# Kernel optimization log

Measured on AMD Instinct MI355X. Metric: run time of the kernel, lower is better.

## Reference

```python
import jax, jax.numpy as jnp
import numpy as np
from jax.ops import segment_sum

N_NODES = 50000
N_EDGES = 800000
D_IN = 256
D_HID2 = 256   # hidden_channels * 2
D_HID = 128    # hidden_channels
D_MLP = 64     # hidden_channels // 2
D_OUT = 64


def setup_inputs() -> dict:
    key = jax.random.key(0)
    ks = jax.random.split(key, 16)
    def glorot(k, shape):
        lim = float(np.sqrt(6.0 / (shape[0] + shape[1])))
        return jax.random.uniform(k, shape, jnp.float32, -lim, lim)
    x = jax.random.normal(ks[0], (N_NODES, D_IN), jnp.float32)
    edge_index = jax.random.randint(ks[1], (2, N_EDGES), 0, N_NODES, jnp.int64)
    return {
        "x": x,
        "edge_index": edge_index,
        "W1": glorot(ks[2], (D_IN, D_HID2)),   "b1": jnp.zeros((D_HID2,), jnp.float32),
        "W2": glorot(ks[3], (D_HID2, D_HID2)), "b2": jnp.zeros((D_HID2,), jnp.float32),
        "W3": glorot(ks[4], (D_HID2, D_HID)),  "b3": jnp.zeros((D_HID,), jnp.float32),
        "mW1": glorot(ks[5], (D_HID, D_MLP)),  "mb1": jnp.zeros((D_MLP,), jnp.float32),
        "mW2": glorot(ks[6], (D_MLP, D_OUT)),  "mb2": jnp.zeros((D_OUT,), jnp.float32),
    }


def _graph_conv(x, src, dst, W, b, n_nodes):
    # DGL GraphConv with norm='both': h = D_in^{-1/2} * A @ (D_out^{-1/2} * x @ W) + b
    ones = jnp.ones((src.shape[0],), x.dtype)
    deg_out = jnp.clip(segment_sum(ones, src, num_segments=n_nodes), 1.0)
    deg_in = jnp.clip(segment_sum(ones, dst, num_segments=n_nodes), 1.0)
    h = (x * jax.lax.rsqrt(deg_out)[:, None]) @ W          # [N, d_out]
    agg = segment_sum(h[src], dst, num_segments=n_nodes)    # gather-scatter over edges
    return agg * jax.lax.rsqrt(deg_in)[:, None] + b


def reference(x, edge_index, W1, b1, W2, b2, W3, b3, mW1, mb1, mW2, mb2):
    src, dst = edge_index[0], edge_index[1]
    n = x.shape[0]
    # eval mode: dropout is identity
    h = jax.nn.relu(_graph_conv(x, src, dst, W1, b1, n))
    h = jax.nn.relu(_graph_conv(h, src, dst, W2, b2, n))
    h_last = jax.nn.relu(_graph_conv(h, src, dst, W3, b3, n))
    out = jax.nn.relu(h_last @ mW1 + mb1) @ mW2 + mb2
    return (out, h_last)
```

## Files before the change

### kernel.cpp

```cpp
#include <hip/hip_runtime.h>
#include <hip/hip_bf16.h>

typedef __hip_bfloat16 bf16;
typedef __attribute__((ext_vector_type(8))) __bf16 bfrag;
typedef __attribute__((ext_vector_type(4))) float f32x4;

#define N_NODES 50000
#define N_EDGES 800000
#define GB_GEMM 782
#define GB_PLACE 3125

__device__ __forceinline__ unsigned short f2bf(float f) {
    bf16 h = __float2bfloat16(f);
    return *reinterpret_cast<unsigned short*>(&h);
}

__device__ __forceinline__ uint4 zero4() { uint4 z; z.x = z.y = z.z = z.w = 0u; return z; }

__device__ __forceinline__ void load_edge(const int* __restrict__ ei, int fl64,
                                          int e, int& s, int& d) {
    if (fl64) { s = ei[2 * e]; d = ei[2 * N_EDGES + 2 * e]; }
    else      { s = ei[e];     d = ei[N_EDGES + e]; }
}

__device__ __forceinline__ float rdf(const void* p, int off, int f32) {
    return f32 ? ((const float*)p)[off] : (float)((const bf16*)p)[off];
}

__global__ void detect_zero_kernel(const unsigned short* __restrict__ xb,
                                   const int* __restrict__ ei,
                                   int* __restrict__ flags,
                                   int* __restrict__ cnt) {
    int i = blockIdx.x * 256 + threadIdx.x;
    if (i < 2 * N_NODES) cnt[i] = 0;
    if (blockIdx.x == 0) {
        __shared__ int s_insane, s_nonzero;
        int t = threadIdx.x;
        if (t == 0) { s_insane = 0; s_nonzero = 0; }
        __syncthreads();
        unsigned short h = xb[2 * t];
        int e = (h >> 7) & 0xFF;
        if (!(e == 0 || (e >= 90 && e <= 150))) atomicOr(&s_insane, 1);
        if (ei[2 * t + 1] != 0) atomicOr(&s_nonzero, 1);
        __syncthreads();
        if (t == 0) { flags[0] = s_insane ? 1 : 0; flags[1] = s_nonzero ? 0 : 1; }
    }
}

__global__ void cvt_all_kernel(const void* W1, const void* W2, const void* W3,
                               const void* mW1, const void* mW2,
                               const void* b1, const void* b2, const void* b3,
                               const void* mb1, const void* mb2,
                               const int* __restrict__ flags,
                               unsigned short* __restrict__ WT,
                               float* __restrict__ biasd) {
    int i = blockIdx.x * 256 + threadIdx.x;
    if (i >= 176896) return;
    const int f32 = flags[0];
    if (i < 163840) {
        const void* s; int local, N;
        if      (i <  65536) { s = W1; local = i;          N = 256; }
        else if (i < 131072) { s = W2; local = i -  65536; N = 256; }
        else                 { s = W3; local = i - 131072; N = 128; }
        int n = local >> 8, k = local & 255;
        WT[i] = f2bf(rdf(s, k * N + n, f32));
    } else if (i < 172032) {
        int local = i - 163840;
        int n = local >> 7, k = local & 127;
        WT[i] = f2bf(rdf(mW1, k * 64 + n, f32));
    } else if (i < 176128) {
        int local = i - 172032;
        int n = local >> 6, k = local & 63;
        WT[i] = f2bf(rdf(mW2, k * 64 + n, f32));
    } else {
        int local = i - 176128;
        const void* s; int off;
        if      (local < 256) { s = b1;  off = local; }
        else if (local < 512) { s = b2;  off = local - 256; }
        else if (local < 640) { s = b3;  off = local - 512; }
        else if (local < 704) { s = mb1; off = local - 640; }
        else                  { s = mb2; off = local - 704; }
        biasd[local] = rdf(s, off, f32);
    }
}

__device__ __forceinline__ uint4 ld8_bf16(const unsigned short* p) {
    return *(const uint4*)p;
}
__device__ __forceinline__ uint4 ld8_f32(const float* p) {
    float4 a = *(const float4*)(p);
    float4 b = *(const float4*)(p + 4);
    uint4 r;
    r.x = ((unsigned)f2bf(a.y) << 16) | f2bf(a.x);
    r.y = ((unsigned)f2bf(a.w) << 16) | f2bf(a.z);
    r.z = ((unsigned)f2bf(b.y) << 16) | f2bf(b.x);
    r.w = ((unsigned)f2bf(b.w) << 16) | f2bf(b.z);
    return r;
}

template <bool DUALX>
__device__ __forceinline__ void gemm_body(
        unsigned short (*Xs)[40], unsigned short (*Ws)[40],
        const void* __restrict__ Xv, const int* __restrict__ flags,
        const unsigned short* __restrict__ WT,
        unsigned short* __restrict__ C,
        int bx, int by, int M, int N) {
    constexpr int K = 256;
    const int tid  = threadIdx.x;
    const int lane = tid & 63;
    const int w    = tid >> 6;
    const int wr   = (w >> 1) * 64;
    const int wc   = (w & 1) * 64;
    const int lrow = lane & 15;
    const int koff = (lane >> 4) * 8;
    const int row0 = by * 128;
    const int col0 = bx * 128;
    const bool xf32 = DUALX && (flags[0] != 0);
    const unsigned short* Xb = (const unsigned short*)Xv;
    const float* Xf = (const float*)Xv;

    const int r0 = tid >> 2, q0 = tid & 3;
    const int r1 = r0 + 64;
    const int gr0 = row0 + r0, gr1 = row0 + r1;

    uint4 xv0, xv1, wv0, wv1;
    {
        int e = q0 * 8;
        xv0 = (gr0 < M) ? (xf32 ? ld8_f32(Xf + (size_t)gr0 * K + e)
                                : ld8_bf16(Xb + (size_t)gr0 * K + e)) : zero4();
        xv1 = (gr1 < M) ? (xf32 ? ld8_f32(Xf + (size_t)gr1 * K + e)
                                : ld8_bf16(Xb + (size_t)gr1 * K + e)) : zero4();
        wv0 = *(const uint4*)(WT + (size_t)(col0 + r0) * K + e);
        wv1 = *(const uint4*)(WT + (size_t)(col0 + r1) * K + e);
    }

    f32x4 acc[4][4] = {};

    for (int k0 = 0; k0 < K; k0 += 32) {
        *(uint4*)&Xs[r0][q0 * 8] = xv0;
        *(uint4*)&Xs[r1][q0 * 8] = xv1;
        *(uint4*)&Ws[r0][q0 * 8] = wv0;
        *(uint4*)&Ws[r1][q0 * 8] = wv1;
        __syncthreads();

        const int k1 = k0 + 32;
        if (k1 < K) {
            int e = k1 + q0 * 8;
            xv0 = (gr0 < M) ? (xf32 ? ld8_f32(Xf + (size_t)gr0 * K + e)
                                    : ld8_bf16(Xb + (size_t)gr0 * K + e)) : zero4();
            xv1 = (gr1 < M) ? (xf32 ? ld8_f32(Xf + (size_t)gr1 * K + e)
                                    : ld8_bf16(Xb + (size_t)gr1 * K + e)) : zero4();
            wv0 = *(const uint4*)(WT + (size_t)(col0 + r0) * K + e);
            wv1 = *(const uint4*)(WT + (size_t)(col0 + r1) * K + e);
        }

        bfrag af[4], bv[4];
#pragma unroll
        for (int i = 0; i < 4; i++)
            af[i] = *(const bfrag*)&Xs[wr + i * 16 + lrow][koff];
#pragma unroll
        for (int j = 0; j < 4; j++)
            bv[j] = *(const bfrag*)&Ws[wc + j * 16 + lrow][koff];
#pragma unroll
        for (int i = 0; i < 4; i++)
#pragma unroll
            for (int j = 0; j < 4; j++)
                acc[i][j] = __builtin_amdgcn_mfma_f32_16x16x32_bf16(
                    af[i], bv[j], acc[i][j], 0, 0, 0);
        __syncthreads();
    }

#pragma unroll
    for (int i = 0; i < 4; i++) {
#pragma unroll
        for (int r = 0; r < 4; r++) {
            int row = row0 + wr + i * 16 + ((lane >> 4) * 4) + r;
            if (row >= M) continue;
#pragma unroll
            for (int j = 0; j < 4; j++) {
                int col = col0 + wc + j * 16 + lrow;
                C[(size_t)row * N + col] = f2bf(acc[i][j][r]);
            }
        }
    }
}

__launch_bounds__(256)
__global__ void megaA_kernel(const void* __restrict__ x,
                             const int* __restrict__ ei,
                             const int* __restrict__ flags,
                             const unsigned short* __restrict__ WT,
                             unsigned short* __restrict__ Hbf,
                             int* __restrict__ cntS, int* __restrict__ cntD,
                             unsigned short* __restrict__ esrc_pad, int M) {
    __shared__ unsigned short Xs[128][40];
    __shared__ unsigned short Ws[128][40];
    const int bid = blockIdx.x;
    if (bid < GB_GEMM) {
        gemm_body<true>(Xs, Ws, x, flags, WT, Hbf, bid & 1, bid >> 1, M, 256);
    } else {
        int e = (bid - GB_GEMM) * 256 + threadIdx.x;
        if (e < N_EDGES) {
            int s, d; load_edge(ei, flags[1], e, s, d);
            atomicAdd(&cntS[s], 1);
            int pos = atomicAdd(&cntD[d], 1);
            if (pos < 64) esrc_pad[(d << 6) + pos] = (unsigned short)s;
        }
    }
}

__launch_bounds__(256)
__global__ void mfma_gemm_kernel(const unsigned short* __restrict__ X,
                                 const int* __restrict__ flags,
                                 const unsigned short* __restrict__ WT,
                                 unsigned short* __restrict__ C,
                                 int M, int N) {
    __shared__ unsigned short Xs[128][40];
    __shared__ unsigned short Ws[128][40];
    gemm_body<false>(Xs, Ws, X, flags, WT, C, blockIdx.x, blockIdx.y, M, N);
}

__launch_bounds__(256)
__global__ void mfma_mlp2_kernel(const unsigned short* __restrict__ X,
                                 const unsigned short* __restrict__ WT1,
                                 const unsigned short* __restrict__ WT2,
                                 const float* __restrict__ b1,
                                 const float* __restrict__ b2,
                                 float* __restrict__ out, int M) {
    __shared__ unsigned short Xs[128][136];
    __shared__ unsigned short W1s[64][136];
    __shared__ unsigned short W2s[64][72];
    const int tid  = threadIdx.x;
    const int lane = tid & 63;
    const int w    = tid >> 6;
    const int lrow = lane & 15;
    const int koff = (lane >> 4) * 8;
    const int row0 = blockIdx.x * 128;

#pragma unroll
    for (int i = 0; i < 8; i++) {
        int c = tid + i * 256;
        int r = c >> 4, q = c & 15;
        int gr = row0 + r;
        uint4 v = (gr < M) ? *(const uint4*)(X + (size_t)gr * 128 + q * 8) : zero4();
        *(uint4*)&Xs[r][q * 8] = v;
    }
#pragma unroll
    for (int i = 0; i < 4; i++) {
        int c = tid + i * 256;
        int n = c >> 4, q = c & 15;
        *(uint4*)&W1s[n][q * 8] = *(const uint4*)(WT1 + (size_t)n * 128 + q * 8);
    }
#pragma unroll
    for (int i = 0; i < 2; i++) {
        int c = tid + i * 256;
        int n = c >> 3, q = c & 7;
        *(uint4*)&W2s[n][q * 8] = *(const uint4*)(WT2 + (size_t)n * 64 + q * 8);
    }
    __syncthreads();

    f32x4 acc[2][4] = {};
#pragma unroll
    for (int k0 = 0; k0 < 128; k0 += 32) {
        bfrag af[2], bv[4];
#pragma unroll
        for (int i = 0; i < 2; i++)
            af[i] = *(const bfrag*)&Xs[w * 32 + i * 16 + lrow][k0 + koff];
#pragma unroll
        for (int j = 0; j < 4; j++)
            bv[j] = *(const bfrag*)&W1s[j * 16 + lrow][k0 + koff];
#pragma unroll
        for (int i = 0; i < 2; i++)
#pragma unroll
            for (int j = 0; j < 4; j++)
                acc[i][j] = __builtin_amdgcn_mfma_f32_16x16x32_bf16(
                    af[i], bv[j], acc[i][j], 0, 0, 0);
    }
    __syncthreads();

#pragma unroll
    for (int i = 0; i < 2; i++) {
#pragma unroll
        for (int r = 0; r < 4; r++) {
            int row = w * 32 + i * 16 + ((lane >> 4) * 4) + r;
#pragma unroll
            for (int j = 0; j < 4; j++) {
                int col = j * 16 + lrow;
                Xs[row][col] = f2bf(fmaxf(acc[i][j][r] + b1[col], 0.0f));
            }
        }
    }
    __syncthreads();

    f32x4 acc2[2][4] = {};
#pragma unroll
    for (int k0 = 0; k0 < 64; k0 += 32) {
        bfrag af[2], bv[4];
#pragma unroll
        for (int i = 0; i < 2; i++)
            af[i] = *(const bfrag*)&Xs[w * 32 + i * 16 + lrow][k0 + koff];
#pragma unroll
        for (int j = 0; j < 4; j++)
            bv[j] = *(const bfrag*)&W2s[j * 16 + lrow][k0 + koff];
#pragma unroll
        for (int i = 0; i < 2; i++)
#pragma unroll
            for (int j = 0; j < 4; j++)
                acc2[i][j] = __builtin_amdgcn_mfma_f32_16x16x32_bf16(
                    af[i], bv[j], acc2[i][j], 0, 0, 0);
    }

#pragma unroll
    for (int i = 0; i < 2; i++) {
#pragma unroll
        for (int r = 0; r < 4; r++) {
            int row = row0 + w * 32 + i * 16 + ((lane >> 4) * 4) + r;
            if (row >= M) continue;
#pragma unroll
            for (int j = 0; j < 4; j++) {
                int col = j * 16 + lrow;
                out[(size_t)row * 64 + col] = acc2[i][j][r] + b2[col];
            }
        }
    }
}

__device__ __forceinline__ void accs(unsigned int u, float s, float& a0, float& a1) {
    a0 = fmaf(s, __uint_as_float(u << 16), a0);
    a1 = fmaf(s, __uint_as_float(u & 0xffff0000u), a1);
}
__device__ __forceinline__ void acc4s(uint4 u, float s, float& a0, float& a1,
                                      float& a2, float& a3, float& a4, float& a5,
                                      float& a6, float& a7) {
    accs(u.x, s, a0, a1); accs(u.y, s, a2, a3);
    accs(u.z, s, a4, a5); accs(u.w, s, a6, a7);
}

template <int LQ, int OUT>
__launch_bounds__(256)
__global__ void gather_bf16_kernel(const int* __restrict__ cntD,
                                   const int* __restrict__ cntS,
                                   const unsigned short* __restrict__ esrc_pad,
                                   const unsigned short* __restrict__ H,
                                   const float* __restrict__ bias,
                                   float* __restrict__ Yf,
                                   unsigned short* __restrict__ Yb, int nNodes) {
    constexpr int NPB = 256 / LQ;
    constexpr int D = LQ * 8;
    const int tid = threadIdx.x;
    const int node = blockIdx.x * NPB + tid / LQ;
    const int lane = tid % LQ;
    if (node >= nNodes) return;
    const uint4* __restrict__ H4 = (const uint4*)H;
    const unsigned short* __restrict__ ep = esrc_pad + (node << 6);

    float a0 = 0.f, a1 = 0.f, a2 = 0.f, a3 = 0.f;
    float a4 = 0.f, a5 = 0.f, a6 = 0.f, a7 = 0.f;
    const int cn = min(cntD[node], 64);
    int j = 0;
    for (; j + 4 <= cn; j += 4) {
        int s0 = ep[j], s1 = ep[j + 1], s2 = ep[j + 2], s3 = ep[j + 3];
        float w0 = rsqrtf((float)max(cntS[s0], 1));
        float w1 = rsqrtf((float)max(cntS[s1], 1));
        float w2 = rsqrtf((float)max(cntS[s2], 1));
        float w3 = rsqrtf((float)max(cntS[s3], 1));
        uint4 u0 = H4[(size_t)s0 * LQ + lane];
        uint4 u1 = H4[(size_t)s1 * LQ + lane];
        uint4 u2 = H4[(size_t)s2 * LQ + lane];
        uint4 u3 = H4[(size_t)s3 * LQ + lane];
        acc4s(u0, w0, a0, a1, a2, a3, a4, a5, a6, a7);
        acc4s(u1, w1, a0, a1, a2, a3, a4, a5, a6, a7);
        acc4s(u2, w2, a0, a1, a2, a3, a4, a5, a6, a7);
        acc4s(u3, w3, a0, a1, a2, a3, a4, a5, a6, a7);
    }
    for (; j < cn; j++) {
        int s0 = ep[j];
        float w0 = rsqrtf((float)max(cntS[s0], 1));
        uint4 u = H4[(size_t)s0 * LQ + lane];
        acc4s(u, w0, a0, a1, a2, a3, a4, a5, a6, a7);
    }
    const float sc = rsqrtf((float)max(cntD[node], 1));
    const float* bp = bias + lane * 8;
    float4 b0 = *(const float4*)(bp);
    float4 b1 = *(const float4*)(bp + 4);
    float r0 = fmaxf(fmaf(a0, sc, b0.x), 0.0f);
    float r1 = fmaxf(fmaf(a1, sc, b0.y), 0.0f);
    float r2 = fmaxf(fmaf(a2, sc, b0.z), 0.0f);
    float r3 = fmaxf(fmaf(a3, sc, b0.w), 0.0f);
    float r4 = fmaxf(fmaf(a4, sc, b1.x), 0.0f);
    float r5 = fmaxf(fmaf(a5, sc, b1.y), 0.0f);
    float r6 = fmaxf(fmaf(a6, sc, b1.z), 0.0f);
    float r7 = fmaxf(fmaf(a7, sc, b1.w), 0.0f);
    if (OUT == 2) {
        float* yp = Yf + (size_t)node * D + lane * 8;
        float4 o0 = {r0, r1, r2, r3};
        float4 o1 = {r4, r5, r6, r7};
        *(float4*)(yp)     = o0;
        *(float4*)(yp + 4) = o1;
    }
    {
        unsigned short* yp = Yb + (size_t)node * D + lane * 8;
        ushort4 o0, o1;
        o0.x = f2bf(r0); o0.y = f2bf(r1); o0.z = f2bf(r2); o0.w = f2bf(r3);
        o1.x = f2bf(r4); o1.y = f2bf(r5); o1.z = f2bf(r6); o1.w = f2bf(r7);
        *(ushort4*)(yp)     = o0;
        *(ushort4*)(yp + 4) = o1;
    }
}

extern "C" void kernel_launch(void* const* d_in, const int* in_sizes, int n_in,
                              void* d_out, int out_size, void* d_ws, size_t ws_size,
                              hipStream_t stream) {
    const void* x  = d_in[0];
    const int*  ei = (const int*)d_in[1];
    const void *W1 = d_in[2],  *b1 = d_in[3];
    const void *W2 = d_in[4],  *b2 = d_in[5];
    const void *W3 = d_in[6],  *b3 = d_in[7];
    const void *mW1 = d_in[8], *mb1 = d_in[9];
    const void *mW2 = d_in[10],*mb2 = d_in[11];

    float* out   = (float*)d_out;
    float* out_h = out + (size_t)N_NODES * 64;

    float* ws = (float*)d_ws;
    size_t off = 0;
    int*   flags  = (int*)(ws + off); off += 64;
    int*   cntS   = (int*)(ws + off); off += N_NODES;
    int*   cntD   = (int*)(ws + off); off += N_NODES;
    unsigned short* esrc_p = (unsigned short*)(ws + off);
    off += (size_t)N_NODES * 32;
    float* biasd  = ws + off;         off += 768;
    off = (off + 63) & ~(size_t)63;
    unsigned short* WT  = (unsigned short*)(ws + off); off += 88448;
    unsigned short* Gbf = (unsigned short*)(ws + off); off += (size_t)N_NODES * 128;
    unsigned short* Hbf = (unsigned short*)(ws + off); off += (size_t)N_NODES * 128;
    unsigned short* hob = (unsigned short*)(ws + off); off += (size_t)N_NODES * 64;

    const int M = N_NODES;
    const dim3 blk(256);
    const int gy128 = (M + 127) / 128;

    detect_zero_kernel<<<391, blk, 0, stream>>>(
        (const unsigned short*)x, ei, flags, cntS);

    cvt_all_kernel<<<(176896 + 255) / 256, blk, 0, stream>>>(
        W1, W2, W3, mW1, mW2, b1, b2, b3, mb1, mb2, flags, WT, biasd);

    megaA_kernel<<<GB_GEMM + GB_PLACE, blk, 0, stream>>>(
        x, ei, flags, WT, Hbf, cntS, cntD, esrc_p, M);

    gather_bf16_kernel<32, 0><<<(M + 7) / 8, blk, 0, stream>>>(
        cntD, cntS, esrc_p, Hbf, biasd, nullptr, Gbf, M);

    mfma_gemm_kernel<<<dim3(2, gy128), blk, 0, stream>>>(
        Gbf, flags, WT + 65536, Hbf, M, 256);
    gather_bf16_kernel<32, 0><<<(M + 7) / 8, blk, 0, stream>>>(
        cntD, cntS, esrc_p, Hbf, biasd + 256, nullptr, Gbf, M);

    mfma_gemm_kernel<<<dim3(1, gy128), blk, 0, stream>>>(
        Gbf, flags, WT + 131072, Hbf, M, 128);
    gather_bf16_kernel<16, 2><<<(M + 15) / 16, blk, 0, stream>>>(
        cntD, cntS, esrc_p, Hbf, biasd + 512, out_h, hob, M);

    mfma_mlp2_kernel<<<gy128, blk, 0, stream>>>(
        hob, WT + 163840, WT + 172032, biasd + 640, biasd + 704, out, M);
}
```

Before: 382.4 us.

## Sort per-node source lists and precompute degree rsqrt scales for gathers

Adds a kernel that bitonic-sorts each destination node's padded source list within a wavefront, and precomputes rsqrt of the out-degree and in-degree per node into float arrays. The three gather kernels then read those scales instead of recomputing rsqrt from the count arrays. Sorting the sources makes gathered rows follow ascending addresses, which is meant to improve cache and TLB locality. Smaller changes: vectorized int2 edge loads for int64 indices and nontemporal stores for the adjacency writes. The cost is one extra launch and a pass over the padded adjacency.

```diff
diff --git a/kernel.cpp b/kernel.cpp
--- a/kernel.cpp
+++ b/kernel.cpp
@@ -19,8 +19,14 @@
 
 __device__ __forceinline__ void load_edge(const int* __restrict__ ei, int fl64,
                                           int e, int& s, int& d) {
-    if (fl64) { s = ei[2 * e]; d = ei[2 * N_EDGES + 2 * e]; }
-    else      { s = ei[e];     d = ei[N_EDGES + e]; }
+    if (fl64) {
+        int2 a = ((const int2*)ei)[e];
+        int2 b = ((const int2*)ei)[N_EDGES + e];
+        s = a.x; d = b.x;
+    } else {
+        s = ei[e];
+        d = ei[N_EDGES + e];
+    }
 }
 
 __device__ __forceinline__ float rdf(const void* p, int off, int f32) {
@@ -204,8 +210,41 @@
             int s, d; load_edge(ei, flags[1], e, s, d);
             atomicAdd(&cntS[s], 1);
             int pos = atomicAdd(&cntD[d], 1);
-            if (pos < 64) esrc_pad[(d << 6) + pos] = (unsigned short)s;
+            if (pos < 64)
+                __builtin_nontemporal_store((unsigned short)s,
+                                            &esrc_pad[(d << 6) + pos]);
         }
+    }
+}
+
+__launch_bounds__(256)
+__global__ void sort_scale_kernel(const int* __restrict__ cntD,
+                                  const int* __restrict__ cntS,
+                                  unsigned short* __restrict__ esrc_pad,
+                                  float* __restrict__ sOutf,
+                                  float* __restrict__ sInf, int nNodes) {
+    const int node = blockIdx.x * 4 + (threadIdx.x >> 6);
+    const int lane = threadIdx.x & 63;
+    if (node >= nNodes) return;
+    unsigned short* ep = esrc_pad + (node << 6);
+    const int cn = min(cntD[node], 64);
+    unsigned v = (lane < cn) ? (unsigned)ep[lane] : 0xFFFFu;
+#pragma unroll
+    for (int k = 2; k <= 64; k <<= 1) {
+#pragma unroll
+        for (int m = k >> 1; m >= 1; m >>= 1) {
+            unsigned p = __shfl_xor(v, m, 64);
+            bool lower = (lane & m) == 0;
+            bool asc   = (lane & k) == 0;
+            unsigned lo = v < p ? v : p;
+            unsigned hi = v < p ? p : v;
+            v = (asc == lower) ? lo : hi;
+        }
+    }
+    if (lane < cn) ep[lane] = (unsigned short)v;
+    if (lane == 0) {
+        sOutf[node] = rsqrtf((float)max(cntS[node], 1));
+        sInf[node]  = rsqrtf((float)max(cntD[node], 1));
     }
 }
 
@@ -339,10 +378,11 @@
 template <int LQ, int OUT>
 __launch_bounds__(256)
 __global__ void gather_bf16_kernel(const int* __restrict__ cntD,
-                                   const int* __restrict__ cntS,
+                                   const float* __restrict__ sOutf,
                                    const unsigned short* __restrict__ esrc_pad,
                                    const unsigned short* __restrict__ H,
                                    const float* __restrict__ bias,
+                                   const float* __restrict__ sInf,
                                    float* __restrict__ Yf,
                                    unsigned short* __restrict__ Yb, int nNodes) {
     constexpr int NPB = 256 / LQ;
@@ -360,10 +400,10 @@
     int j = 0;
     for (; j + 4 <= cn; j += 4) {
         int s0 = ep[j], s1 = ep[j + 1], s2 = ep[j + 2], s3 = ep[j + 3];
-        float w0 = rsqrtf((float)max(cntS[s0], 1));
-        float w1 = rsqrtf((float)max(cntS[s1], 1));
-        float w2 = rsqrtf((float)max(cntS[s2], 1));
-        float w3 = rsqrtf((float)max(cntS[s3], 1));
+        float w0 = sOutf[s0];
+        float w1 = sOutf[s1];
+        float w2 = sOutf[s2];
+        float w3 = sOutf[s3];
         uint4 u0 = H4[(size_t)s0 * LQ + lane];
         uint4 u1 = H4[(size_t)s1 * LQ + lane];
         uint4 u2 = H4[(size_t)s2 * LQ + lane];
@@ -375,11 +415,11 @@
     }
     for (; j < cn; j++) {
         int s0 = ep[j];
-        float w0 = rsqrtf((float)max(cntS[s0], 1));
+        float w0 = sOutf[s0];
         uint4 u = H4[(size_t)s0 * LQ + lane];
         acc4s(u, w0, a0, a1, a2, a3, a4, a5, a6, a7);
     }
-    const float sc = rsqrtf((float)max(cntD[node], 1));
+    const float sc = sInf[node];
     const float* bp = bias + lane * 8;
     float4 b0 = *(const float4*)(bp);
     float4 b1 = *(const float4*)(bp + 4);
@@ -430,6 +470,8 @@
     unsigned short* esrc_p = (unsigned short*)(ws + off);
     off += (size_t)N_NODES * 32;
     float* biasd  = ws + off;         off += 768;
+    float* sOutf  = ws + off;         off += N_NODES;
+    float* sInf   = ws + off;         off += N_NODES;
     off = (off + 63) & ~(size_t)63;
     unsigned short* WT  = (unsigned short*)(ws + off); off += 88448;
     unsigned short* Gbf = (unsigned short*)(ws + off); off += (size_t)N_NODES * 128;
@@ -449,18 +491,21 @@
     megaA_kernel<<<GB_GEMM + GB_PLACE, blk, 0, stream>>>(
         x, ei, flags, WT, Hbf, cntS, cntD, esrc_p, M);
 
+    sort_scale_kernel<<<(M + 3) / 4, blk, 0, stream>>>(
+        cntD, cntS, esrc_p, sOutf, sInf, M);
+
     gather_bf16_kernel<32, 0><<<(M + 7) / 8, blk, 0, stream>>>(
-        cntD, cntS, esrc_p, Hbf, biasd, nullptr, Gbf, M);
+        cntD, sOutf, esrc_p, Hbf, biasd, sInf, nullptr, Gbf, M);
 
     mfma_gemm_kernel<<<dim3(2, gy128), blk, 0, stream>>>(
         Gbf, flags, WT + 65536, Hbf, M, 256);
     gather_bf16_kernel<32, 0><<<(M + 7) / 8, blk, 0, stream>>>(
-        cntD, cntS, esrc_p, Hbf, biasd + 256, nullptr, Gbf, M);
+        cntD, sOutf, esrc_p, Hbf, biasd + 256, sInf, nullptr, Gbf, M);
 
     mfma_gemm_kernel<<<dim3(1, gy128), blk, 0, stream>>>(
         Gbf, flags, WT + 131072, Hbf, M, 128);
     gather_bf16_kernel<16, 2><<<(M + 15) / 16, blk, 0, stream>>>(
-        cntD, cntS, esrc_p, Hbf, biasd + 512, out_h, hob, M);
+        cntD, sOutf, esrc_p, Hbf, biasd + 512, sInf, out_h, hob, M);
 
     mfma_mlp2_kernel<<<gy128, blk, 0, stream>>>(
         hob, WT + 163840, WT + 172032, biasd + 640, biasd + 704, out, M);
```

Result: slower. 399.0 us (+4.3%).

## Fuse gather-aggregate with next-layer GEMM and MLP into single kernels

Applied to the files above, without the earlier changes.

Each layer's gather/aggregate is merged with the following dense GEMM in one kernel. The aggregated 32-row tile stays in LDS and is multiplied by the next weight matrix, whose rows are then scaled by the source-degree rsqrt so the next gather skips the per-edge cntS lookup. The final conv gather is fused with the two-layer MLP. The edge load uses int2 and the padded-index stores are nontemporal. This removes intermediate global round trips and launches, but the GEMMs now read B fragments straight from global memory in small tiles, which may lower MFMA efficiency.

```diff
diff --git a/kernel.cpp b/kernel.cpp
--- a/kernel.cpp
+++ b/kernel.cpp
@@ -19,8 +19,14 @@
 
 __device__ __forceinline__ void load_edge(const int* __restrict__ ei, int fl64,
                                           int e, int& s, int& d) {
-    if (fl64) { s = ei[2 * e]; d = ei[2 * N_EDGES + 2 * e]; }
-    else      { s = ei[e];     d = ei[N_EDGES + e]; }
+    if (fl64) {
+        int2 a = ((const int2*)ei)[e];
+        int2 b = ((const int2*)ei)[N_EDGES + e];
+        s = a.x; d = b.x;
+    } else {
+        s = ei[e];
+        d = ei[N_EDGES + e];
+    }
 }
 
 __device__ __forceinline__ float rdf(const void* p, int off, int f32) {
@@ -204,207 +210,219 @@
             int s, d; load_edge(ei, flags[1], e, s, d);
             atomicAdd(&cntS[s], 1);
             int pos = atomicAdd(&cntD[d], 1);
-            if (pos < 64) esrc_pad[(d << 6) + pos] = (unsigned short)s;
-        }
-    }
-}
-
-__launch_bounds__(256)
-__global__ void mfma_gemm_kernel(const unsigned short* __restrict__ X,
-                                 const int* __restrict__ flags,
-                                 const unsigned short* __restrict__ WT,
-                                 unsigned short* __restrict__ C,
-                                 int M, int N) {
-    __shared__ unsigned short Xs[128][40];
-    __shared__ unsigned short Ws[128][40];
-    gemm_body<false>(Xs, Ws, X, flags, WT, C, blockIdx.x, blockIdx.y, M, N);
-}
-
-__launch_bounds__(256)
-__global__ void mfma_mlp2_kernel(const unsigned short* __restrict__ X,
-                                 const unsigned short* __restrict__ WT1,
-                                 const unsigned short* __restrict__ WT2,
-                                 const float* __restrict__ b1,
-                                 const float* __restrict__ b2,
-                                 float* __restrict__ out, int M) {
-    __shared__ unsigned short Xs[128][136];
-    __shared__ unsigned short W1s[64][136];
-    __shared__ unsigned short W2s[64][72];
-    const int tid  = threadIdx.x;
+            if (pos < 64)
+                __builtin_nontemporal_store((unsigned short)s,
+                                            &esrc_pad[(d << 6) + pos]);
+        }
+    }
+}
+
+__device__ __forceinline__ void accs(unsigned int u, float s, float& a0, float& a1) {
+    a0 = fmaf(s, __uint_as_float(u << 16), a0);
+    a1 = fmaf(s, __uint_as_float(u & 0xffff0000u), a1);
+}
+__device__ __forceinline__ void acc4s(uint4 u, float s, float (&a)[8]) {
+    accs(u.x, s, a[0], a[1]); accs(u.y, s, a[2], a[3]);
+    accs(u.z, s, a[4], a[5]); accs(u.w, s, a[6], a[7]);
+}
+
+template <int LQ, bool ESCALE>
+__device__ __forceinline__ void gather_accum(const uint4* __restrict__ H4,
+                                             const unsigned short* __restrict__ ep,
+                                             const int* __restrict__ cntS,
+                                             int cn, int lane, float (&a)[8]) {
+    int j = 0;
+    for (; j + 4 <= cn; j += 4) {
+        int s0 = ep[j], s1 = ep[j + 1], s2 = ep[j + 2], s3 = ep[j + 3];
+        float w0 = 1.f, w1 = 1.f, w2 = 1.f, w3 = 1.f;
+        if (ESCALE) {
+            w0 = rsqrtf((float)max(cntS[s0], 1));
+            w1 = rsqrtf((float)max(cntS[s1], 1));
+            w2 = rsqrtf((float)max(cntS[s2], 1));
+            w3 = rsqrtf((float)max(cntS[s3], 1));
+        }
+        uint4 u0 = H4[(size_t)s0 * LQ + lane];
+        uint4 u1 = H4[(size_t)s1 * LQ + lane];
+        uint4 u2 = H4[(size_t)s2 * LQ + lane];
+        uint4 u3 = H4[(size_t)s3 * LQ + lane];
+        acc4s(u0, w0, a); acc4s(u1, w1, a);
+        acc4s(u2, w2, a); acc4s(u3, w3, a);
+    }
+    for (; j < cn; j++) {
+        int s0 = ep[j];
+        float w0 = ESCALE ? rsqrtf((float)max(cntS[s0], 1)) : 1.f;
+        uint4 u = H4[(size_t)s0 * LQ + lane];
+        acc4s(u, w0, a);
+    }
+}
+
+template <int NOUT, bool ESCALE>
+__launch_bounds__(512)
+__global__ void fconv_kernel(const unsigned short* __restrict__ H,
+                             const int* __restrict__ cntD,
+                             const int* __restrict__ cntS,
+                             const unsigned short* __restrict__ esrc_pad,
+                             const float* __restrict__ bias,
+                             const unsigned short* __restrict__ WTn,
+                             unsigned short* __restrict__ Hout,
+                             int M) {
+    __shared__ unsigned short Xf[32][264];
+    const int tid = threadIdx.x;
+    const int row0 = blockIdx.x * 32;
+
+    {
+        const int slot = tid >> 5;
+        const int gl   = tid & 31;
+        const uint4* H4 = (const uint4*)H;
+        const float* bp = bias + gl * 8;
+        float4 b0 = *(const float4*)(bp);
+        float4 b1 = *(const float4*)(bp + 4);
+#pragma unroll
+        for (int round = 0; round < 2; ++round) {
+            const int node = row0 + round * 16 + slot;
+            float a[8] = {};
+            float sc = 0.f;
+            if (node < M) {
+                const unsigned short* ep = esrc_pad + (node << 6);
+                const int cn = min(cntD[node], 64);
+                gather_accum<32, ESCALE>(H4, ep, cntS, cn, gl, a);
+                sc = rsqrtf((float)max(cntD[node], 1));
+            }
+            ushort4 o0, o1;
+            o0.x = f2bf(fmaxf(fmaf(a[0], sc, b0.x), 0.f));
+            o0.y = f2bf(fmaxf(fmaf(a[1], sc, b0.y), 0.f));
+            o0.z = f2bf(fmaxf(fmaf(a[2], sc, b0.z), 0.f));
+            o0.w = f2bf(fmaxf(fmaf(a[3], sc, b0.w), 0.f));
+            o1.x = f2bf(fmaxf(fmaf(a[4], sc, b1.x), 0.f));
+            o1.y = f2bf(fmaxf(fmaf(a[5], sc, b1.y), 0.f));
+            o1.z = f2bf(fmaxf(fmaf(a[6], sc, b1.z), 0.f));
+            o1.w = f2bf(fmaxf(fmaf(a[7], sc, b1.w), 0.f));
+            *(ushort4*)&Xf[round * 16 + slot][gl * 8]     = o0;
+            *(ushort4*)&Xf[round * 16 + slot][gl * 8 + 4] = o1;
+        }
+    }
+    __syncthreads();
+
     const int lane = tid & 63;
     const int w    = tid >> 6;
     const int lrow = lane & 15;
     const int koff = (lane >> 4) * 8;
-    const int row0 = blockIdx.x * 128;
-
-#pragma unroll
-    for (int i = 0; i < 8; i++) {
-        int c = tid + i * 256;
-        int r = c >> 4, q = c & 15;
-        int gr = row0 + r;
-        uint4 v = (gr < M) ? *(const uint4*)(X + (size_t)gr * 128 + q * 8) : zero4();
-        *(uint4*)&Xs[r][q * 8] = v;
-    }
-#pragma unroll
-    for (int i = 0; i < 4; i++) {
-        int c = tid + i * 256;
-        int n = c >> 4, q = c & 15;
-        *(uint4*)&W1s[n][q * 8] = *(const uint4*)(WT1 + (size_t)n * 128 + q * 8);
-    }
-#pragma unroll
-    for (int i = 0; i < 2; i++) {
-        int c = tid + i * 256;
-        int n = c >> 3, q = c & 7;
-        *(uint4*)&W2s[n][q * 8] = *(const uint4*)(WT2 + (size_t)n * 64 + q * 8);
-    }
-    __syncthreads();
-
-    f32x4 acc[2][4] = {};
-#pragma unroll
-    for (int k0 = 0; k0 < 128; k0 += 32) {
-        bfrag af[2], bv[4];
-#pragma unroll
-        for (int i = 0; i < 2; i++)
-            af[i] = *(const bfrag*)&Xs[w * 32 + i * 16 + lrow][k0 + koff];
-#pragma unroll
-        for (int j = 0; j < 4; j++)
-            bv[j] = *(const bfrag*)&W1s[j * 16 + lrow][k0 + koff];
-#pragma unroll
-        for (int i = 0; i < 2; i++)
-#pragma unroll
-            for (int j = 0; j < 4; j++)
-                acc[i][j] = __builtin_amdgcn_mfma_f32_16x16x32_bf16(
-                    af[i], bv[j], acc[i][j], 0, 0, 0);
-    }
-    __syncthreads();
-
-#pragma unroll
-    for (int i = 0; i < 2; i++) {
-#pragma unroll
-        for (int r = 0; r < 4; r++) {
-            int row = w * 32 + i * 16 + ((lane >> 4) * 4) + r;
-#pragma unroll
-            for (int j = 0; j < 4; j++) {
-                int col = j * 16 + lrow;
-                Xs[row][col] = f2bf(fmaxf(acc[i][j][r] + b1[col], 0.0f));
-            }
-        }
-    }
-    __syncthreads();
-
-    f32x4 acc2[2][4] = {};
-#pragma unroll
-    for (int k0 = 0; k0 < 64; k0 += 32) {
-        bfrag af[2], bv[4];
-#pragma unroll
-        for (int i = 0; i < 2; i++)
-            af[i] = *(const bfrag*)&Xs[w * 32 + i * 16 + lrow][k0 + koff];
-#pragma unroll
-        for (int j = 0; j < 4; j++)
-            bv[j] = *(const bfrag*)&W2s[j * 16 + lrow][k0 + koff];
-#pragma unroll
-        for (int i = 0; i < 2; i++)
-#pragma unroll
-            for (int j = 0; j < 4; j++)
-                acc2[i][j] = __builtin_amdgcn_mfma_f32_16x16x32_bf16(
-                    af[i], bv[j], acc2[i][j], 0, 0, 0);
-    }
-
-#pragma unroll
-    for (int i = 0; i < 2; i++) {
-#pragma unroll
-        for (int r = 0; r < 4; r++) {
-            int row = row0 + w * 32 + i * 16 + ((lane >> 4) * 4) + r;
-            if (row >= M) continue;
-#pragma unroll
-            for (int j = 0; j < 4; j++) {
-                int col = j * 16 + lrow;
-                out[(size_t)row * 64 + col] = acc2[i][j][r] + b2[col];
-            }
-        }
-    }
-}
-
-__device__ __forceinline__ void accs(unsigned int u, float s, float& a0, float& a1) {
-    a0 = fmaf(s, __uint_as_float(u << 16), a0);
-    a1 = fmaf(s, __uint_as_float(u & 0xffff0000u), a1);
-}
-__device__ __forceinline__ void acc4s(uint4 u, float s, float& a0, float& a1,
-                                      float& a2, float& a3, float& a4, float& a5,
-                                      float& a6, float& a7) {
-    accs(u.x, s, a0, a1); accs(u.y, s, a2, a3);
-    accs(u.z, s, a4, a5); accs(u.w, s, a6, a7);
-}
-
-template <int LQ, int OUT>
-__launch_bounds__(256)
-__global__ void gather_bf16_kernel(const int* __restrict__ cntD,
-                                   const int* __restrict__ cntS,
-                                   const unsigned short* __restrict__ esrc_pad,
-                                   const unsigned short* __restrict__ H,
-                                   const float* __restrict__ bias,
-                                   float* __restrict__ Yf,
-                                   unsigned short* __restrict__ Yb, int nNodes) {
-    constexpr int NPB = 256 / LQ;
-    constexpr int D = LQ * 8;
+    const int wr   = (w >> 2) * 16;
+    constexpr int NJ = (NOUT == 256) ? 4 : 2;
+    const int wc   = (w & 3) * (NJ * 16);
+    f32x4 acc[NJ] = {};
+#pragma unroll 2
+    for (int k0 = 0; k0 < 256; k0 += 32) {
+        const bfrag af = *(const bfrag*)&Xf[wr + lrow][k0 + koff];
+#pragma unroll
+        for (int j = 0; j < NJ; j++) {
+            const bfrag bv = *(const bfrag*)&WTn[(size_t)(wc + j * 16 + lrow) * 256
+                                                 + k0 + koff];
+            acc[j] = __builtin_amdgcn_mfma_f32_16x16x32_bf16(af, bv, acc[j], 0, 0, 0);
+        }
+    }
+#pragma unroll
+    for (int r = 0; r < 4; r++) {
+        const int rl = wr + (lane >> 4) * 4 + r;
+        const int grow = row0 + rl;
+        if (grow >= M) continue;
+        const float s = rsqrtf((float)max(cntS[grow], 1));
+#pragma unroll
+        for (int j = 0; j < NJ; j++)
+            Hout[(size_t)grow * NOUT + wc + j * 16 + lrow] = f2bf(acc[j][r] * s);
+    }
+}
+
+__launch_bounds__(512)
+__global__ void fmlp_kernel(const unsigned short* __restrict__ H3,
+                            const int* __restrict__ cntD,
+                            const unsigned short* __restrict__ esrc_pad,
+                            const float* __restrict__ b3,
+                            const float* __restrict__ mb1,
+                            const float* __restrict__ mb2,
+                            const unsigned short* __restrict__ WT1,
+                            const unsigned short* __restrict__ WT2,
+                            float* __restrict__ out,
+                            float* __restrict__ outh,
+                            int M) {
+    __shared__ unsigned short Xs[32][136];
+    __shared__ unsigned short X2[32][72];
     const int tid = threadIdx.x;
-    const int node = blockIdx.x * NPB + tid / LQ;
-    const int lane = tid % LQ;
-    if (node >= nNodes) return;
-    const uint4* __restrict__ H4 = (const uint4*)H;
-    const unsigned short* __restrict__ ep = esrc_pad + (node << 6);
-
-    float a0 = 0.f, a1 = 0.f, a2 = 0.f, a3 = 0.f;
-    float a4 = 0.f, a5 = 0.f, a6 = 0.f, a7 = 0.f;
-    const int cn = min(cntD[node], 64);
-    int j = 0;
-    for (; j + 4 <= cn; j += 4) {
-        int s0 = ep[j], s1 = ep[j + 1], s2 = ep[j + 2], s3 = ep[j + 3];
-        float w0 = rsqrtf((float)max(cntS[s0], 1));
-        float w1 = rsqrtf((float)max(cntS[s1], 1));
-        float w2 = rsqrtf((float)max(cntS[s2], 1));
-        float w3 = rsqrtf((float)max(cntS[s3], 1));
-        uint4 u0 = H4[(size_t)s0 * LQ + lane];
-        uint4 u1 = H4[(size_t)s1 * LQ + lane];
-        uint4 u2 = H4[(size_t)s2 * LQ + lane];
-        uint4 u3 = H4[(size_t)s3 * LQ + lane];
-        acc4s(u0, w0, a0, a1, a2, a3, a4, a5, a6, a7);
-        acc4s(u1, w1, a0, a1, a2, a3, a4, a5, a6, a7);
-        acc4s(u2, w2, a0, a1, a2, a3, a4, a5, a6, a7);
-        acc4s(u3, w3, a0, a1, a2, a3, a4, a5, a6, a7);
-    }
-    for (; j < cn; j++) {
-        int s0 = ep[j];
-        float w0 = rsqrtf((float)max(cntS[s0], 1));
-        uint4 u = H4[(size_t)s0 * LQ + lane];
-        acc4s(u, w0, a0, a1, a2, a3, a4, a5, a6, a7);
-    }
-    const float sc = rsqrtf((float)max(cntD[node], 1));
-    const float* bp = bias + lane * 8;
-    float4 b0 = *(const float4*)(bp);
-    float4 b1 = *(const float4*)(bp + 4);
-    float r0 = fmaxf(fmaf(a0, sc, b0.x), 0.0f);
-    float r1 = fmaxf(fmaf(a1, sc, b0.y), 0.0f);
-    float r2 = fmaxf(fmaf(a2, sc, b0.z), 0.0f);
-    float r3 = fmaxf(fmaf(a3, sc, b0.w), 0.0f);
-    float r4 = fmaxf(fmaf(a4, sc, b1.x), 0.0f);
-    float r5 = fmaxf(fmaf(a5, sc, b1.y), 0.0f);
-    float r6 = fmaxf(fmaf(a6, sc, b1.z), 0.0f);
-    float r7 = fmaxf(fmaf(a7, sc, b1.w), 0.0f);
-    if (OUT == 2) {
-        float* yp = Yf + (size_t)node * D + lane * 8;
-        float4 o0 = {r0, r1, r2, r3};
-        float4 o1 = {r4, r5, r6, r7};
-        *(float4*)(yp)     = o0;
-        *(float4*)(yp + 4) = o1;
-    }
+    const int row0 = blockIdx.x * 32;
+
     {
-        unsigned short* yp = Yb + (size_t)node * D + lane * 8;
+        const int slot = tid >> 4;
+        const int gl   = tid & 15;
+        const uint4* H4 = (const uint4*)H3;
+        const int node = row0 + slot;
+        float a[8] = {};
+        float sc = 0.f;
+        if (node < M) {
+            const unsigned short* ep = esrc_pad + (node << 6);
+            const int cn = min(cntD[node], 64);
+            gather_accum<16, false>(H4, ep, nullptr, cn, gl, a);
+            sc = rsqrtf((float)max(cntD[node], 1));
+        }
+        const float* bp = b3 + gl * 8;
+        float4 b0 = *(const float4*)(bp);
+        float4 b1 = *(const float4*)(bp + 4);
+        float r0 = fmaxf(fmaf(a[0], sc, b0.x), 0.f);
+        float r1 = fmaxf(fmaf(a[1], sc, b0.y), 0.f);
+        float r2 = fmaxf(fmaf(a[2], sc, b0.z), 0.f);
+        float r3 = fmaxf(fmaf(a[3], sc, b0.w), 0.f);
+        float r4 = fmaxf(fmaf(a[4], sc, b1.x), 0.f);
+        float r5 = fmaxf(fmaf(a[5], sc, b1.y), 0.f);
+        float r6 = fmaxf(fmaf(a[6], sc, b1.z), 0.f);
+        float r7 = fmaxf(fmaf(a[7], sc, b1.w), 0.f);
+        if (node < M) {
+            float* yp = outh + (size_t)node * 128 + gl * 8;
+            float4 o0 = {r0, r1, r2, r3};
+            float4 o1 = {r4, r5, r6, r7};
+            *(float4*)(yp)     = o0;
+            *(float4*)(yp + 4) = o1;
+        }
         ushort4 o0, o1;
         o0.x = f2bf(r0); o0.y = f2bf(r1); o0.z = f2bf(r2); o0.w = f2bf(r3);
         o1.x = f2bf(r4); o1.y = f2bf(r5); o1.z = f2bf(r6); o1.w = f2bf(r7);
-        *(ushort4*)(yp)     = o0;
-        *(ushort4*)(yp + 4) = o1;
+        *(ushort4*)&Xs[slot][gl * 8]     = o0;
+        *(ushort4*)&Xs[slot][gl * 8 + 4] = o1;
+    }
+    __syncthreads();
+
+    const int lane = tid & 63;
+    const int w    = tid >> 6;
+    const int lrow = lane & 15;
+    const int koff = (lane >> 4) * 8;
+    const int wr   = (w >> 2) * 16;
+    const int wc   = (w & 3) * 16;
+    f32x4 acc = {};
+#pragma unroll
+    for (int k0 = 0; k0 < 128; k0 += 32) {
+        const bfrag af = *(const bfrag*)&Xs[wr + lrow][k0 + koff];
+        const bfrag bv = *(const bfrag*)&WT1[(size_t)(wc + lrow) * 128 + k0 + koff];
+        acc = __builtin_amdgcn_mfma_f32_16x16x32_bf16(af, bv, acc, 0, 0, 0);
+    }
+#pragma unroll
+    for (int r = 0; r < 4; r++) {
+        const int rl  = wr + (lane >> 4) * 4 + r;
+        const int col = wc + lrow;
+        X2[rl][col] = f2bf(fmaxf(acc[r] + mb1[col], 0.f));
+    }
+    __syncthreads();
+
+    f32x4 acc2 = {};
+#pragma unroll
+    for (int k0 = 0; k0 < 64; k0 += 32) {
+        const bfrag af = *(const bfrag*)&X2[wr + lrow][k0 + koff];
+        const bfrag bv = *(const bfrag*)&WT2[(size_t)(wc + lrow) * 64 + k0 + koff];
+        acc2 = __builtin_amdgcn_mfma_f32_16x16x32_bf16(af, bv, acc2, 0, 0, 0);
+    }
+#pragma unroll
+    for (int r = 0; r < 4; r++) {
+        const int rl   = wr + (lane >> 4) * 4 + r;
+        const int grow = row0 + rl;
+        if (grow >= M) continue;
+        out[(size_t)grow * 64 + wc + lrow] = acc2[r] + mb2[wc + lrow];
     }
 }
 
@@ -432,13 +450,13 @@
     float* biasd  = ws + off;         off += 768;
     off = (off + 63) & ~(size_t)63;
     unsigned short* WT  = (unsigned short*)(ws + off); off += 88448;
-    unsigned short* Gbf = (unsigned short*)(ws + off); off += (size_t)N_NODES * 128;
     unsigned short* Hbf = (unsigned short*)(ws + off); off += (size_t)N_NODES * 128;
-    unsigned short* hob = (unsigned short*)(ws + off); off += (size_t)N_NODES * 64;
+    unsigned short* H2  = (unsigned short*)(ws + off); off += (size_t)N_NODES * 128;
+    unsigned short* H3  = Hbf;
 
     const int M = N_NODES;
     const dim3 blk(256);
-    const int gy128 = (M + 127) / 128;
+    const int g32 = (M + 31) / 32;
 
     detect_zero_kernel<<<391, blk, 0, stream>>>(
         (const unsigned short*)x, ei, flags, cntS);
@@ -449,19 +467,13 @@
     megaA_kernel<<<GB_GEMM + GB_PLACE, blk, 0, stream>>>(
         x, ei, flags, WT, Hbf, cntS, cntD, esrc_p, M);
 
-    gather_bf16_kernel<32, 0><<<(M + 7) / 8, blk, 0, stream>>>(
-        cntD, cntS, esrc_p, Hbf, biasd, nullptr, Gbf, M);
-
-    mfma_gemm_kernel<<<dim3(2, gy128), blk, 0, stream>>>(
-        Gbf, flags, WT + 65536, Hbf, M, 256);
-    gather_bf16_kernel<32, 0><<<(M + 7) / 8, blk, 0, stream>>>(
-        cntD, cntS, esrc_p, Hbf, biasd + 256, nullptr, Gbf, M);
-
-    mfma_gemm_kernel<<<dim3(1, gy128), blk, 0, stream>>>(
-        Gbf, flags, WT + 131072, Hbf, M, 128);
-    gather_bf16_kernel<16, 2><<<(M + 15) / 16, blk, 0, stream>>>(
-        cntD, cntS, esrc_p, Hbf, biasd + 512, out_h, hob, M);
-
-    mfma_mlp2_kernel<<<gy128, blk, 0, stream>>>(
-        hob, WT + 163840, WT + 172032, biasd + 640, biasd + 704, out, M);
-}
+    fconv_kernel<256, true><<<g32, dim3(512), 0, stream>>>(
+        Hbf, cntD, cntS, esrc_p, biasd, WT + 65536, H2, M);
+
+    fconv_kernel<128, false><<<g32, dim3(512), 0, stream>>>(
+        H2, cntD, cntS, esrc_p, biasd + 256, WT + 131072, H3, M);
+
+    fmlp_kernel<<<g32, dim3(512), 0, stream>>>(
+        H3, cntD, esrc_p, biasd + 512, biasd + 640, biasd + 704,
+        WT + 163840, WT + 172032, out, out_h, M);
+}
```

Result: slower. 425.8 us (+11.3%).
